# Kernel optimization log

Hardware: AMD Instinct MI355X
Metric: run time of the kernel (lower is better)

The kernel has to match this reference:

```python
import jax, jax.numpy as jnp
import numpy as np

WS = 8
NH = 8
C = 192
HD = C // NH
SCALE = HD ** -0.5
EPS = 1e-5


def setup_inputs() -> dict:
    key = jax.random.key(0)
    ks = jax.random.split(key, 7)
    B, H, W = 8, 256, 256
    x = jax.random.normal(ks[0], (B, C, H, W), dtype=jnp.float32)
    gamma = jnp.ones((C,), dtype=jnp.float32)
    beta = jnp.zeros((C,), dtype=jnp.float32)
    w_qkv = jax.random.normal(ks[1], (C, 3 * C), dtype=jnp.float32) * (C ** -0.5)
    b_qkv = jnp.zeros((3 * C,), dtype=jnp.float32)
    w_proj = jax.random.normal(ks[2], (C, C), dtype=jnp.float32) * (C ** -0.5)
    b_proj = jnp.zeros((C,), dtype=jnp.float32)
    return {"x": x, "gamma": gamma, "beta": beta, "w_qkv": w_qkv,
            "b_qkv": b_qkv, "w_proj": w_proj, "b_proj": b_proj}


def reference(x, gamma, beta, w_qkv, b_qkv, w_proj, b_proj):
    B, Cc, H, W = x.shape
    # H, W chosen divisible by WS -> pad branch is a no-op
    nh, nw = H // WS, W // WS
    # window partition: [B,C,H,W] -> [B*nh*nw, WS*WS, C]
    xw = x.reshape(B, Cc, nh, WS, nw, WS)
    xw = xw.transpose(0, 2, 4, 3, 5, 1).reshape(-1, WS * WS, Cc)
    # LayerNorm over channel dim
    mu = xw.mean(axis=-1, keepdims=True)
    var = jnp.mean((xw - mu) ** 2, axis=-1, keepdims=True)
    xn = (xw - mu) * jax.lax.rsqrt(var + EPS) * gamma + beta
    # QKV projection -> [3, nWin, NH, S, HD]
    S = WS * WS
    qkv = (xn @ w_qkv + b_qkv).reshape(-1, S, 3, NH, HD)
    qkv = qkv.transpose(2, 0, 3, 1, 4)
    q, k, v = qkv[0], qkv[1], qkv[2]
    attn = jax.nn.softmax(jnp.einsum('whsd,whtd->whst', q, k) * SCALE, axis=-1)
    xa = jnp.einsum('whst,whtd->whsd', attn, v)
    xa = xa.transpose(0, 2, 1, 3).reshape(-1, S, Cc)
    xa = xa @ w_proj + b_proj
    # un-window: -> [B, C, H, W]
    xa = xa.reshape(B, nh, nw, WS, WS, Cc)
    xa = xa.transpose(0, 5, 1, 3, 2, 4).reshape(B, Cc, H, W)
    return jax.nn.sigmoid(xa.mean(axis=1, keepdims=True))
```

## Files before the change

### kernel.cpp

```cpp
#include <hip/hip_runtime.h>
#include <hip/hip_bf16.h>


typedef __attribute__((ext_vector_type(4))) float floatx4;
typedef __attribute__((ext_vector_type(8))) short short8;

#define SCALE_Q 0.20412414523193154f
#define LN_EPS 1e-5f

#define RXN 200
#define OFF_XN 0
#define OFF_Q  25600
#define OFF_K  51200
#define OFF_VW 76800
#define LDS_BYTES 78848

__device__ __forceinline__ floatx4 mfma16(short8 a, short8 b, floatx4 c) {
  return __builtin_amdgcn_mfma_f32_16x16x32_bf16(a, b, c, 0, 0, 0);
}

__global__ void prep_kernel(const float* __restrict__ w_qkv,
                            const float* __restrict__ w_proj,
                            const float* __restrict__ b_proj,
                            __hip_bfloat16* __restrict__ wfrag,
                            float* __restrict__ wbar) {
  int tid = blockIdx.x * 256 + threadIdx.x;
  if (tid < 36 * 6 * 64) {
    int j = tid / 384, rem = tid % 384, ksr = rem / 64, l = rem % 64;
    int n  = 16 * j + (l & 15);
    int k0 = 32 * ksr + (l >> 4) * 8;
#pragma unroll
    for (int i = 0; i < 8; ++i)
      wfrag[(size_t)tid * 8 + i] = __float2bfloat16(w_qkv[(k0 + i) * 576 + n]);
  }
  if (tid < 192) {
    float s = 0.f;
    for (int c = 0; c < 192; ++c) s += w_proj[tid * 192 + c];
    wbar[tid] = s * (1.f / 192.f);
  } else if (tid == 192) {
    float s = 0.f;
    for (int c = 0; c < 192; ++c) s += b_proj[c];
    wbar[192] = s * (1.f / 192.f);
  }
}

__global__ __launch_bounds__(512, 2) void swin_kernel(
    const float* __restrict__ x,
    const float* __restrict__ gamma,
    const float* __restrict__ beta,
    const float* __restrict__ b_qkv,
    const __hip_bfloat16* __restrict__ wfrag,
    const float* __restrict__ wbar,
    float* __restrict__ out) {
  __shared__ __align__(16) char smem[LDS_BYTES];
  __hip_bfloat16* xn = (__hip_bfloat16*)(smem + OFF_XN);
  __hip_bfloat16* lq = (__hip_bfloat16*)(smem + OFF_Q);
  __hip_bfloat16* lk = (__hip_bfloat16*)(smem + OFF_K);
  float* vwf = (float*)(smem + OFF_VW);
  float2* scratch = (float2*)(smem + OFF_Q);

  const int tid = threadIdx.x;
  const int w   = tid >> 6;
  const int l   = tid & 63;
  const int l15 = l & 15;
  const int lg  = l >> 4;
  const int mi  = w & 3;
  const int jh  = w >> 2;
  const floatx4 fzero = {0.f, 0.f, 0.f, 0.f};
  const short8 zero8 = {0, 0, 0, 0, 0, 0, 0, 0};

  const int p    = blockIdx.x;
  const int bb   = p & 7;
  const int wh   = (p >> 3) & 31;
  const int hseg = p >> 8;
  const int tr = l >> 3, tc = l & 7;
  const int c0 = w * 24;
  const float* xb = x + (size_t)bb * 192 * 65536 + (size_t)(wh * 8 + tr) * 256
                      + hseg * 128 + tc;

  float xr[24];
#pragma unroll
  for (int i = 0; i < 24; ++i) xr[i] = xb[(size_t)(c0 + i) * 65536];

#pragma unroll 1
  for (int it = 0; it < 16; ++it) {
    float s1 = 0.f, s2 = 0.f;
#pragma unroll
    for (int i = 0; i < 24; ++i) { s1 += xr[i]; s2 += xr[i] * xr[i]; }
    scratch[w * 64 + l] = make_float2(s1, s2);
    __syncthreads();
    float ts = 0.f, tq = 0.f;
#pragma unroll
    for (int g = 0; g < 8; ++g) { float2 v = scratch[g * 64 + l]; ts += v.x; tq += v.y; }
    vwf[tid] = 0.f;
    const float mu   = ts * (1.f / 192.f);
    const float rstd = rsqrtf(tq * (1.f / 192.f) - mu * mu + LN_EPS);
    {
      short8 pk[3];
#pragma unroll
      for (int i = 0; i < 24; ++i) {
        float xv = (xr[i] - mu) * rstd * gamma[c0 + i] + beta[c0 + i];
        __hip_bfloat16 hb = __float2bfloat16(xv);
        short sv; __builtin_memcpy(&sv, &hb, 2);
        pk[i >> 3][i & 7] = sv;
      }
#pragma unroll
      for (int q2 = 0; q2 < 3; ++q2)
        *(short8*)&xn[l * RXN + c0 + q2 * 8] = pk[q2];
    }
    __syncthreads();

    short8 af[6];
#pragma unroll
    for (int ks = 0; ks < 6; ++ks)
      af[ks] = *(const short8*)&xn[(16 * mi + l15) * RXN + 32 * ks + lg * 8];

    auto gemm = [&](int j) -> floatx4 {
      floatx4 aa = fzero;
      const short8* bp = (const short8*)wfrag + (size_t)(j * 384 + l);
#pragma unroll
      for (int ks = 0; ks < 6; ++ks)
        aa = mfma16(af[ks], bp[ks * 64], aa);
      return aa;
    };
    auto kwrite = [&](int j, floatx4 aa) {
      const int cc = 16 * j + l15 - 192;
      const int hh = cc / 24, dd = cc - hh * 24;
      const float bias = b_qkv[16 * j + l15];
#pragma unroll
      for (int rg = 0; rg < 4; ++rg) {
        int t = 16 * mi + lg * 4 + rg;
        lk[t * RXN + hh * 24 + dd] = __float2bfloat16(aa[rg] + bias);
      }
    };

    if (jh == 0) {
#pragma unroll 2
      for (int j = 0; j < 12; ++j) {
        floatx4 aa = gemm(j);
        const int n = 16 * j + l15;
        const int hh = n / 24, dd = n - hh * 24;
        const float bias = b_qkv[n];
#pragma unroll
        for (int rg = 0; rg < 4; ++rg) {
          int t = 16 * mi + lg * 4 + rg;
          lq[t * RXN + hh * 24 + dd] = __float2bfloat16((aa[rg] + bias) * SCALE_Q);
        }
      }
#pragma unroll 2
      for (int j = 12; j < 18; ++j) kwrite(j, gemm(j));
    } else {
#pragma unroll 2
      for (int j = 18; j < 24; ++j) kwrite(j, gemm(j));
#pragma unroll 2
      for (int j = 24; j < 36; ++j) {
        floatx4 aa = gemm(j);
        const int cc = 16 * j + l15 - 384;
        const int hh = cc / 24;
        const float wbv = wbar[cc];
        const float bias = b_qkv[16 * j + l15];
        float part[4];
#pragma unroll
        for (int rg = 0; rg < 4; ++rg)
          part[rg] = (aa[rg] + bias) * wbv;
#pragma unroll
        for (int rg = 0; rg < 4; ++rg) {
          float t0 = part[rg];
          t0 += __shfl_xor(t0, 1);
          t0 += __shfl_xor(t0, 2);
          t0 += __shfl_xor(t0, 4);
          part[rg] = t0;
        }
        if ((l15 & 7) == 0)
#pragma unroll
          for (int rg = 0; rg < 4; ++rg) {
            int t = 16 * mi + lg * 4 + rg;
            atomicAdd(&vwf[hh * 64 + t], part[rg]);
          }
      }
    }
    __syncthreads();

    {
      const int hh = w;
      short8 kf[4];
#pragma unroll
      for (int j2 = 0; j2 < 4; ++j2)
        kf[j2] = (lg < 3)
                   ? *(const short8*)&lk[(16 * j2 + l15) * RXN + hh * 24 + lg * 8]
                   : zero8;
      float vwv[4];
#pragma unroll
      for (int j2 = 0; j2 < 4; ++j2) vwv[j2] = vwf[hh * 64 + 16 * j2 + l15];

#pragma unroll
      for (int i = 0; i < 4; ++i) {
        short8 qf = (lg < 3)
                      ? *(const short8*)&lq[(16 * i + l15) * RXN + hh * 24 + lg * 8]
                      : zero8;
        floatx4 sc[4];
#pragma unroll
        for (int j2 = 0; j2 < 4; ++j2)
          sc[j2] = mfma16(qf, kf[j2], fzero);
        float num[4] = {0.f, 0.f, 0.f, 0.f};
        float den[4] = {0.f, 0.f, 0.f, 0.f};
#pragma unroll
        for (int j2 = 0; j2 < 4; ++j2)
#pragma unroll
          for (int rg = 0; rg < 4; ++rg) {
            float pv = exp2f(sc[j2][rg] * 1.44269504f);
            den[rg] += pv;
            num[rg] = fmaf(pv, vwv[j2], num[rg]);
          }
#pragma unroll
        for (int m = 1; m < 16; m <<= 1)
#pragma unroll
          for (int rg = 0; rg < 4; ++rg) {
            num[rg] += __shfl_xor(num[rg], m);
            den[rg] += __shfl_xor(den[rg], m);
          }
#pragma unroll
        for (int rg = 0; rg < 4; ++rg)
          if (l15 == i * 4 + rg)
            vwf[hh * 64 + 16 * i + lg * 4 + rg] = __fdividef(num[rg], den[rg]);
      }
    }
    __syncthreads();

    if (it < 15) {
#pragma unroll
      for (int i = 0; i < 24; ++i)
        xr[i] = xb[(size_t)(c0 + i) * 65536 + (it + 1) * 8];
    }

    if (tid < 64) {
      float vL = wbar[192];
#pragma unroll
      for (int h8 = 0; h8 < 8; ++h8) vL += vwf[h8 * 64 + tid];
      out[(size_t)bb * 65536 + (size_t)(wh * 8 + (tid >> 3)) * 256
          + hseg * 128 + it * 8 + (tid & 7)] = 1.f / (1.f + __expf(-vL));
    }
  }
}

extern "C" void kernel_launch(void* const* d_in, const int* in_sizes, int n_in,
                              void* d_out, int out_size, void* d_ws, size_t ws_size,
                              hipStream_t stream) {
  const float* x      = (const float*)d_in[0];
  const float* gamma  = (const float*)d_in[1];
  const float* beta   = (const float*)d_in[2];
  const float* w_qkv  = (const float*)d_in[3];
  const float* b_qkv  = (const float*)d_in[4];
  const float* w_proj = (const float*)d_in[5];
  const float* b_proj = (const float*)d_in[6];
  float* out = (float*)d_out;

  __hip_bfloat16* wfrag = (__hip_bfloat16*)d_ws;
  float* wbar = (float*)((char*)d_ws + 221184);

  prep_kernel<<<54, 256, 0, stream>>>(w_qkv, w_proj, b_proj, wfrag, wbar);
  swin_kernel<<<512, 512, 0, stream>>>(x, gamma, beta, b_qkv, wfrag, wbar, out);
}
```

Baseline: 1.306 ms.

## Retile QKV GEMM to share B fragments across two M tiles and shrink LDS

Each wave now computes two 16-row M tiles against one loaded weight fragment, halving weight-fragment global loads per MFMA, and the 36 output column tiles are split evenly into 9 per wave pair. The Q buffer now aliases the xn buffer (behind an extra barrier) and the scratch is moved, cutting LDS from about 77KB to 52KB, which may allow more resident blocks per CU. The log2e factor is folded into the Q scale, so the softmax exp2 drops one multiply. Gamma and beta are loaded as float4. Keeping twice as many A fragments raises register pressure.

```diff
diff --git a/kernel.cpp b/kernel.cpp
--- a/kernel.cpp
+++ b/kernel.cpp
@@ -5,15 +5,14 @@
 typedef __attribute__((ext_vector_type(4))) float floatx4;
 typedef __attribute__((ext_vector_type(8))) short short8;
 
-#define SCALE_Q 0.20412414523193154f
+#define SCALE_QL2 0.29448889f
 #define LN_EPS 1e-5f
 
 #define RXN 200
 #define OFF_XN 0
-#define OFF_Q  25600
-#define OFF_K  51200
-#define OFF_VW 76800
-#define LDS_BYTES 78848
+#define OFF_K  25600
+#define OFF_VW 51200
+#define LDS_BYTES 53248
 
 __device__ __forceinline__ floatx4 mfma16(short8 a, short8 b, floatx4 c) {
   return __builtin_amdgcn_mfma_f32_16x16x32_bf16(a, b, c, 0, 0, 0);
@@ -54,18 +53,18 @@
     float* __restrict__ out) {
   __shared__ __align__(16) char smem[LDS_BYTES];
   __hip_bfloat16* xn = (__hip_bfloat16*)(smem + OFF_XN);
-  __hip_bfloat16* lq = (__hip_bfloat16*)(smem + OFF_Q);
+  __hip_bfloat16* lq = (__hip_bfloat16*)(smem + OFF_XN);
   __hip_bfloat16* lk = (__hip_bfloat16*)(smem + OFF_K);
   float* vwf = (float*)(smem + OFF_VW);
-  float2* scratch = (float2*)(smem + OFF_Q);
+  float2* scratch = (float2*)(smem + OFF_K);
 
   const int tid = threadIdx.x;
   const int w   = tid >> 6;
   const int l   = tid & 63;
   const int l15 = l & 15;
   const int lg  = l >> 4;
-  const int mi  = w & 3;
-  const int jh  = w >> 2;
+  const int mi2 = w & 1;
+  const int jq  = w >> 1;
   const floatx4 fzero = {0.f, 0.f, 0.f, 0.f};
   const short8 zero8 = {0, 0, 0, 0, 0, 0, 0, 0};
 
@@ -96,13 +95,22 @@
     const float mu   = ts * (1.f / 192.f);
     const float rstd = rsqrtf(tq * (1.f / 192.f) - mu * mu + LN_EPS);
     {
+      const float4* g4 = (const float4*)(gamma + c0);
+      const float4* b4 = (const float4*)(beta + c0);
       short8 pk[3];
 #pragma unroll
-      for (int i = 0; i < 24; ++i) {
-        float xv = (xr[i] - mu) * rstd * gamma[c0 + i] + beta[c0 + i];
-        __hip_bfloat16 hb = __float2bfloat16(xv);
-        short sv; __builtin_memcpy(&sv, &hb, 2);
-        pk[i >> 3][i & 7] = sv;
+      for (int i4 = 0; i4 < 6; ++i4) {
+        float4 gv = g4[i4], bv = b4[i4];
+        float gg[4] = {gv.x, gv.y, gv.z, gv.w};
+        float bbv[4] = {bv.x, bv.y, bv.z, bv.w};
+#pragma unroll
+        for (int q2 = 0; q2 < 4; ++q2) {
+          int i = 4 * i4 + q2;
+          float xv = (xr[i] - mu) * rstd * gg[q2] + bbv[q2];
+          __hip_bfloat16 hb = __float2bfloat16(xv);
+          short sv; __builtin_memcpy(&sv, &hb, 2);
+          pk[i >> 3][i & 7] = sv;
+        }
       }
 #pragma unroll
       for (int q2 = 0; q2 < 3; ++q2)
@@ -110,73 +118,72 @@
     }
     __syncthreads();
 
-    short8 af[6];
-#pragma unroll
-    for (int ks = 0; ks < 6; ++ks)
-      af[ks] = *(const short8*)&xn[(16 * mi + l15) * RXN + 32 * ks + lg * 8];
-
-    auto gemm = [&](int j) -> floatx4 {
-      floatx4 aa = fzero;
+    short8 af[2][6];
+#pragma unroll
+    for (int m2 = 0; m2 < 2; ++m2)
+#pragma unroll
+      for (int ks = 0; ks < 6; ++ks)
+        af[m2][ks] = *(const short8*)
+            &xn[(32 * mi2 + 16 * m2 + l15) * RXN + 32 * ks + lg * 8];
+    __syncthreads();
+
+#pragma unroll 1
+    for (int j = jq * 9; j < jq * 9 + 9; ++j) {
+      floatx4 aa[2] = {fzero, fzero};
       const short8* bp = (const short8*)wfrag + (size_t)(j * 384 + l);
 #pragma unroll
-      for (int ks = 0; ks < 6; ++ks)
-        aa = mfma16(af[ks], bp[ks * 64], aa);
-      return aa;
-    };
-    auto kwrite = [&](int j, floatx4 aa) {
-      const int cc = 16 * j + l15 - 192;
-      const int hh = cc / 24, dd = cc - hh * 24;
-      const float bias = b_qkv[16 * j + l15];
-#pragma unroll
-      for (int rg = 0; rg < 4; ++rg) {
-        int t = 16 * mi + lg * 4 + rg;
-        lk[t * RXN + hh * 24 + dd] = __float2bfloat16(aa[rg] + bias);
-      }
-    };
-
-    if (jh == 0) {
-#pragma unroll 2
-      for (int j = 0; j < 12; ++j) {
-        floatx4 aa = gemm(j);
-        const int n = 16 * j + l15;
+      for (int ks = 0; ks < 6; ++ks) {
+        short8 bf = bp[ks * 64];
+        aa[0] = mfma16(af[0][ks], bf, aa[0]);
+        aa[1] = mfma16(af[1][ks], bf, aa[1]);
+      }
+      const int n = 16 * j + l15;
+      const float bias = b_qkv[n];
+      if (j < 12) {
         const int hh = n / 24, dd = n - hh * 24;
-        const float bias = b_qkv[n];
-#pragma unroll
-        for (int rg = 0; rg < 4; ++rg) {
-          int t = 16 * mi + lg * 4 + rg;
-          lq[t * RXN + hh * 24 + dd] = __float2bfloat16((aa[rg] + bias) * SCALE_Q);
-        }
-      }
-#pragma unroll 2
-      for (int j = 12; j < 18; ++j) kwrite(j, gemm(j));
-    } else {
-#pragma unroll 2
-      for (int j = 18; j < 24; ++j) kwrite(j, gemm(j));
-#pragma unroll 2
-      for (int j = 24; j < 36; ++j) {
-        floatx4 aa = gemm(j);
-        const int cc = 16 * j + l15 - 384;
+#pragma unroll
+        for (int m2 = 0; m2 < 2; ++m2)
+#pragma unroll
+          for (int rg = 0; rg < 4; ++rg) {
+            int t = 32 * mi2 + 16 * m2 + lg * 4 + rg;
+            lq[t * RXN + hh * 24 + dd] =
+                __float2bfloat16((aa[m2][rg] + bias) * SCALE_QL2);
+          }
+      } else if (j < 24) {
+        const int cc = n - 192;
+        const int hh = cc / 24, dd = cc - hh * 24;
+#pragma unroll
+        for (int m2 = 0; m2 < 2; ++m2)
+#pragma unroll
+          for (int rg = 0; rg < 4; ++rg) {
+            int t = 32 * mi2 + 16 * m2 + lg * 4 + rg;
+            lk[t * RXN + hh * 24 + dd] = __float2bfloat16(aa[m2][rg] + bias);
+          }
+      } else {
+        const int cc = n - 384;
         const int hh = cc / 24;
         const float wbv = wbar[cc];
-        const float bias = b_qkv[16 * j + l15];
-        float part[4];
-#pragma unroll
-        for (int rg = 0; rg < 4; ++rg)
-          part[rg] = (aa[rg] + bias) * wbv;
-#pragma unroll
-        for (int rg = 0; rg < 4; ++rg) {
-          float t0 = part[rg];
-          t0 += __shfl_xor(t0, 1);
-          t0 += __shfl_xor(t0, 2);
-          t0 += __shfl_xor(t0, 4);
-          part[rg] = t0;
+#pragma unroll
+        for (int m2 = 0; m2 < 2; ++m2) {
+          float part[4];
+#pragma unroll
+          for (int rg = 0; rg < 4; ++rg)
+            part[rg] = (aa[m2][rg] + bias) * wbv;
+#pragma unroll
+          for (int rg = 0; rg < 4; ++rg) {
+            float t0 = part[rg];
+            t0 += __shfl_xor(t0, 1);
+            t0 += __shfl_xor(t0, 2);
+            t0 += __shfl_xor(t0, 4);
+            part[rg] = t0;
+          }
+          if ((l15 & 7) == 0)
+#pragma unroll
+            for (int rg = 0; rg < 4; ++rg) {
+              int t = 32 * mi2 + 16 * m2 + lg * 4 + rg;
+              atomicAdd(&vwf[hh * 64 + t], part[rg]);
+            }
         }
-        if ((l15 & 7) == 0)
-#pragma unroll
-          for (int rg = 0; rg < 4; ++rg) {
-            int t = 16 * mi + lg * 4 + rg;
-            atomicAdd(&vwf[hh * 64 + t], part[rg]);
-          }
       }
     }
     __syncthreads();
@@ -208,7 +215,7 @@
         for (int j2 = 0; j2 < 4; ++j2)
 #pragma unroll
           for (int rg = 0; rg < 4; ++rg) {
-            float pv = exp2f(sc[j2][rg] * 1.44269504f);
+            float pv = exp2f(sc[j2][rg]);
             den[rg] += pv;
             num[rg] = fmaf(pv, vwv[j2], num[rg]);
           }
```

Result: faster. 1.192 ms (-8.7%).
